# Kernel tuning notes

Hardware: AMD Instinct MI355X
Metric: run time of the kernel (lower is better)

The kernel has to match this reference:

```python
import jax, jax.numpy as jnp
import numpy as np

N_NODES = 100000
N_EDGES = 1600000
D_IN = 64
D_H = 64


def setup_inputs() -> dict:
    key = jax.random.key(0)
    ks = jax.random.split(key, 8)
    inp = {
        "in_feat": jax.random.normal(ks[0], (N_NODES, D_IN), dtype=jnp.float32),
        "src": jax.random.randint(ks[1], (N_EDGES,), 0, N_NODES, dtype=jnp.int64)
        if jax.config.jax_enable_x64
        else jax.random.randint(ks[1], (N_EDGES,), 0, N_NODES).astype(jnp.int32),
        "dst": jax.random.randint(ks[2], (N_EDGES,), 0, N_NODES).astype(jnp.int32),
        "W_self1": jax.random.normal(ks[3], (D_H, D_IN), dtype=jnp.float32) * 0.1,
        "W_neigh1": jax.random.normal(ks[4], (D_H, D_IN), dtype=jnp.float32) * 0.1,
        "b1": jnp.zeros((D_H,), dtype=jnp.float32),
        "W_self2": jax.random.normal(ks[5], (D_H, D_H), dtype=jnp.float32) * 0.1,
        "W_neigh2": jax.random.normal(ks[6], (D_H, D_H), dtype=jnp.float32) * 0.1,
        "b2": jnp.zeros((D_H,), dtype=jnp.float32),
    }
    inp["src"] = inp["src"].astype(jnp.int32)
    return inp


def _sage_mean(x, src, dst, W_self, W_neigh, b, n_nodes):
    # mean aggregation over incoming edges: gather src feats, segment-sum at dst
    msg_sum = jax.ops.segment_sum(x[src], dst, num_segments=n_nodes)  # [N, D]
    deg = jax.ops.segment_sum(jnp.ones_like(dst, dtype=x.dtype), dst, num_segments=n_nodes)
    h_neigh = msg_sum / jnp.maximum(deg, 1.0)[:, None]
    # DGL SAGEConv: fc_self(h) + fc_neigh(h_neigh) + bias
    return x @ W_self.T + h_neigh @ W_neigh.T + b


def reference(in_feat, src, dst, W_self1, W_neigh1, b1, W_self2, W_neigh2, b2):
    n = in_feat.shape[0]
    h = _sage_mean(in_feat, src, dst, W_self1, W_neigh1, b1, n)
    # dropout in eval mode is identity; then relu
    h = jax.nn.relu(h)
    h = _sage_mean(h, src, dst, W_self2, W_neigh2, b2, n)
    return h
```

## Files before the change

### kernel.cpp

```cpp
#include <hip/hip_runtime.h>

#define NN 100000
#define NE 1600000
#define NROWS 100032
#define CAP 48
#define ZOFF (NN * 64)
#define NRANGE 12500
#define SCAT_GROUPS 8
#define SCAT_CHUNKS 196
#define SCAT_EPB 8192
#define SCAT_BLKS (SCAT_GROUPS * SCAT_CHUNKS)
#define CAST_BLKS 6250
#define WCAT_BLKS 64
#define ZCUR_BLKS 391
#define AGG_BLKS 1563

typedef __attribute__((ext_vector_type(8))) short short8;
typedef __attribute__((ext_vector_type(4))) float float4v;
typedef __attribute__((ext_vector_type(4))) int int4v;

__device__ inline unsigned short f2bf(float f)
{
    union { float f; unsigned u; } v; v.f = f;
    unsigned r = v.u + 0x7FFF + ((v.u >> 16) & 1);
    return (unsigned short)(r >> 16);
}
__device__ inline float bf2f(unsigned short h)
{
    union { unsigned u; float f; } v; v.u = ((unsigned)h) << 16; return v.f;
}

__global__ __launch_bounds__(256) void prepA_kernel(
    const float* __restrict__ x,
    const float* __restrict__ Ws1, const float* __restrict__ Wn1,
    const float* __restrict__ Ws2, const float* __restrict__ Wn2,
    unsigned short* __restrict__ XF,
    unsigned short* __restrict__ W1, unsigned short* __restrict__ W2,
    int* __restrict__ cur)
{
    const int b = blockIdx.x;
    const int tid = threadIdx.x;
    if (b < CAST_BLKS) {
        int t = b * 256 + tid;
        int n = t >> 4;
        int k4 = (t & 15) * 4;
        float4v v = __builtin_nontemporal_load(
            (const float4v*)(x + (size_t)n * 64 + k4));
        ushort4 o;
        o.x = f2bf(v[0]); o.y = f2bf(v[1]); o.z = f2bf(v[2]); o.w = f2bf(v[3]);
        *(ushort4*)(XF + (size_t)n * 64 + k4) = o;
    } else if (b < CAST_BLKS + WCAT_BLKS) {
        int id = (b - CAST_BLKS) * 256 + tid;
        int l = id >> 13;
        int r = id & 8191;
        int o = r >> 7, k = r & 127;
        const float* Ws = l ? Ws2 : Ws1;
        const float* Wn = l ? Wn2 : Wn1;
        float v = (k < 64) ? Ws[o * 64 + k] : Wn[o * 64 + (k - 64)];
        (l ? W2 : W1)[r] = f2bf(v);
    } else if (b < CAST_BLKS + WCAT_BLKS + 1) {
        ushort4 z; z.x = 0; z.y = 0; z.z = 0; z.w = 0;
        for (int i = tid; i < 512; i += 256)
            *(ushort4*)(XF + (size_t)NN * 64 + i * 4) = z;
    } else {
        int i = (b - CAST_BLKS - WCAT_BLKS - 1) * 256 + tid;
        if (i < NN) cur[i] = 0;
    }
}

__global__ __launch_bounds__(256) void scatter_kernel(
    const int* __restrict__ src, const int* __restrict__ dst,
    int* __restrict__ cur, int* __restrict__ colb)
{
    const int b = blockIdx.x;
    const int tid = threadIdx.x;
    const int g = b & 7;
    const int chunk = b >> 3;
    const int lo = g * NRANGE;
    const int hi = lo + NRANGE;
    const int base = chunk * SCAT_EPB;
    #pragma unroll
    for (int k = 0; k < 8; ++k) {
        int e = base + (k * 256 + tid) * 4;
        if (e < NE) {
            int4v s4 = __builtin_nontemporal_load((const int4v*)(src + e));
            int4v d4 = __builtin_nontemporal_load((const int4v*)(dst + e));
            int p;
            if (d4[0] >= lo && d4[0] < hi) {
                p = atomicAdd(&cur[d4[0]], 1);
                if (p < CAP) colb[(size_t)d4[0] * CAP + p] = s4[0] << 6;
            }
            if (d4[1] >= lo && d4[1] < hi) {
                p = atomicAdd(&cur[d4[1]], 1);
                if (p < CAP) colb[(size_t)d4[1] * CAP + p] = s4[1] << 6;
            }
            if (d4[2] >= lo && d4[2] < hi) {
                p = atomicAdd(&cur[d4[2]], 1);
                if (p < CAP) colb[(size_t)d4[2] * CAP + p] = s4[2] << 6;
            }
            if (d4[3] >= lo && d4[3] < hi) {
                p = atomicAdd(&cur[d4[3]], 1);
                if (p < CAP) colb[(size_t)d4[3] * CAP + p] = s4[3] << 6;
            }
        }
    }
}

template <int LAYER1>
__global__ __launch_bounds__(256) void aggdense_kernel(
    const unsigned short* __restrict__ XIN,
    const int* __restrict__ cur,
    const int* __restrict__ colb,
    const unsigned short* __restrict__ Wcat,
    const float* __restrict__ bias,
    unsigned short* __restrict__ xout,
    float* __restrict__ fout)
{
    __shared__ __align__(16) unsigned short HN[64 * 72];
    const int tid = threadIdx.x;
    const int wave = tid >> 6;
    const int lane = tid & 63;
    const int g = lane >> 4;
    const int q = lane & 15;
    const int nbase = blockIdx.x * 64 + wave * 16;

    int cntv = (lane < 16 && nbase + lane < NN) ? cur[nbase + lane] : 0;

    int cnt_nx = __shfl(cntv, 0, 64);
    int cc_nx = min(cnt_nx, CAP);
    int ci_nx = (nbase < NN && lane < cc_nx) ? colb[(size_t)nbase * CAP + lane] : ZOFF;

    for (int i = 0; i < 16; ++i) {
        int n = nbase + i;
        int cnt = cnt_nx, cc = cc_nx, ci = ci_nx;
        if (i < 15) {
            cnt_nx = __shfl(cntv, i + 1, 64);
            cc_nx = min(cnt_nx, CAP);
            ci_nx = ((n + 1) < NN && lane < cc_nx)
                      ? colb[(size_t)(n + 1) * CAP + lane] : ZOFF;
        }
        if (n < NN) {
            float a0 = 0.f, a1 = 0.f, a2 = 0.f, a3 = 0.f;
            for (int t = 0; t < cc; t += 16) {
                int i0 = __shfl(ci, t + g, 64);
                int i1 = __shfl(ci, t + 4 + g, 64);
                int i2 = __shfl(ci, t + 8 + g, 64);
                int i3 = __shfl(ci, t + 12 + g, 64);
                ushort4 v0 = *(const ushort4*)(XIN + i0 + q * 4);
                ushort4 v1 = *(const ushort4*)(XIN + i1 + q * 4);
                ushort4 v2 = *(const ushort4*)(XIN + i2 + q * 4);
                ushort4 v3 = *(const ushort4*)(XIN + i3 + q * 4);
                a0 += bf2f(v0.x) + bf2f(v1.x) + bf2f(v2.x) + bf2f(v3.x);
                a1 += bf2f(v0.y) + bf2f(v1.y) + bf2f(v2.y) + bf2f(v3.y);
                a2 += bf2f(v0.z) + bf2f(v1.z) + bf2f(v2.z) + bf2f(v3.z);
                a3 += bf2f(v0.w) + bf2f(v1.w) + bf2f(v2.w) + bf2f(v3.w);
            }
            a0 += __shfl_xor(a0, 16, 64); a0 += __shfl_xor(a0, 32, 64);
            a1 += __shfl_xor(a1, 16, 64); a1 += __shfl_xor(a1, 32, 64);
            a2 += __shfl_xor(a2, 16, 64); a2 += __shfl_xor(a2, 32, 64);
            a3 += __shfl_xor(a3, 16, 64); a3 += __shfl_xor(a3, 32, 64);
            float rdeg = 1.0f / fmaxf((float)cnt, 1.0f);
            if (g == 0) {
                ushort4 o;
                o.x = f2bf(a0 * rdeg); o.y = f2bf(a1 * rdeg);
                o.z = f2bf(a2 * rdeg); o.w = f2bf(a3 * rdeg);
                *(ushort4*)(&HN[(wave * 16 + i) * 72 + q * 4]) = o;
            }
        }
    }
    __syncthreads();

    const int mrow = lane & 15;
    const int kb = lane >> 4;
    const int row0 = nbase;

    short8 a[4];
    {
        const short* ax = (const short*)XIN + (size_t)(row0 + mrow) * 64 + kb * 8;
        const short* ah = (const short*)HN + (wave * 16 + mrow) * 72 + kb * 8;
        a[0] = *(const short8*)(ax);
        a[1] = *(const short8*)(ax + 32);
        a[2] = *(const short8*)(ah);
        a[3] = *(const short8*)(ah + 32);
    }

    float4v acc[4];
    #pragma unroll
    for (int c = 0; c < 4; ++c) acc[c] = (float4v){0.f, 0.f, 0.f, 0.f};

    #pragma unroll
    for (int c = 0; c < 4; ++c) {
        const short* brow = (const short*)Wcat + (c * 16 + mrow) * 128 + kb * 8;
        #pragma unroll
        for (int i = 0; i < 4; ++i) {
            short8 bfr = *(const short8*)(brow + i * 32);
            acc[c] = __builtin_amdgcn_mfma_f32_16x16x32_bf16(a[i], bfr, acc[c], 0, 0, 0);
        }
    }

    const int rbase = row0 + (lane >> 4) * 4;
    #pragma unroll
    for (int c = 0; c < 4; ++c) {
        int o = c * 16 + mrow;
        float bv = bias[o];
        #pragma unroll
        for (int r = 0; r < 4; ++r) {
            int node = rbase + r;
            float val = acc[c][r] + bv;
            if (LAYER1) {
                float h = (node < NN) ? fmaxf(val, 0.f) : 0.f;
                xout[(size_t)node * 64 + o] = f2bf(h);
            } else {
                if (node < NN) fout[(size_t)node * 64 + o] = val;
            }
        }
    }
}

extern "C" void kernel_launch(void* const* d_in, const int* in_sizes, int n_in,
                              void* d_out, int out_size, void* d_ws, size_t ws_size,
                              hipStream_t stream)
{
    const float* in_feat = (const float*)d_in[0];
    const int*   src     = (const int*)d_in[1];
    const int*   dst     = (const int*)d_in[2];
    const float* Ws1     = (const float*)d_in[3];
    const float* Wn1     = (const float*)d_in[4];
    const float* b1      = (const float*)d_in[5];
    const float* Ws2     = (const float*)d_in[6];
    const float* Wn2     = (const float*)d_in[7];
    const float* b2      = (const float*)d_in[8];
    float* out = (float*)d_out;

    int* cur  = (int*)d_ws;
    int* colb = cur + NN;
    unsigned short* XF = (unsigned short*)(colb + (size_t)NN * CAP);
    unsigned short* H1 = XF + (size_t)NROWS * 64;
    unsigned short* W1 = H1 + (size_t)NROWS * 64;
    unsigned short* W2 = W1 + 8192;

    prepA_kernel<<<CAST_BLKS + WCAT_BLKS + 1 + ZCUR_BLKS, 256, 0, stream>>>(
        in_feat, Ws1, Wn1, Ws2, Wn2, XF, W1, W2, cur);

    scatter_kernel<<<SCAT_BLKS, 256, 0, stream>>>(src, dst, cur, colb);

    aggdense_kernel<1><<<AGG_BLKS, 256, 0, stream>>>(
        XF, cur, colb, W1, b1, H1, nullptr);

    aggdense_kernel<0><<<AGG_BLKS, 256, 0, stream>>>(
        H1, cur, colb, W2, b2, nullptr, out);
}
```

Measured before the change: 260.9 us.

## Merge scatter with cast kernel and halve nodes per aggregation block

Zeroing of the degree counters moves into its own small kernel, and the edge scatter runs in the same launch as the feature/weight bf16 cast, so the scatter and cast overlap instead of running as two serial launches. The aggregation kernel now handles 32 nodes per block (8 per wave) with twice as many blocks. This is meant to improve load balance and latency hiding for the irregular gather. Only two of the four waves do the MFMA dense step, leaving half the waves idle in that phase. Bounds checks are dropped because 100000 divides evenly by 32.

Measured after the change: 251.7 us. 3.5% less time.

```diff
diff --git a/kernel.cpp b/kernel.cpp
--- a/kernel.cpp
+++ b/kernel.cpp
@@ -13,7 +13,7 @@
 #define CAST_BLKS 6250
 #define WCAT_BLKS 64
 #define ZCUR_BLKS 391
-#define AGG_BLKS 1563
+#define AGG_BLKS 3125
 
 typedef __attribute__((ext_vector_type(8))) short short8;
 typedef __attribute__((ext_vector_type(4))) float float4v;
@@ -30,18 +30,56 @@
     union { unsigned u; float f; } v; v.u = ((unsigned)h) << 16; return v.f;
 }
 
-__global__ __launch_bounds__(256) void prepA_kernel(
+__global__ __launch_bounds__(256) void zero_kernel(int* __restrict__ cur)
+{
+    int i = blockIdx.x * 256 + threadIdx.x;
+    if (i < NN) cur[i] = 0;
+}
+
+__global__ __launch_bounds__(256) void prep_kernel(
     const float* __restrict__ x,
     const float* __restrict__ Ws1, const float* __restrict__ Wn1,
     const float* __restrict__ Ws2, const float* __restrict__ Wn2,
-    unsigned short* __restrict__ XF,
+    const int* __restrict__ src, const int* __restrict__ dst,
+    unsigned short* __restrict__ XF, unsigned short* __restrict__ H1,
     unsigned short* __restrict__ W1, unsigned short* __restrict__ W2,
-    int* __restrict__ cur)
+    int* __restrict__ cur, int* __restrict__ colb)
 {
     const int b = blockIdx.x;
     const int tid = threadIdx.x;
-    if (b < CAST_BLKS) {
-        int t = b * 256 + tid;
+    if (b < SCAT_BLKS) {
+        const int g = b & 7;
+        const int chunk = b >> 3;
+        const int lo = g * NRANGE;
+        const int hi = lo + NRANGE;
+        const int base = chunk * SCAT_EPB;
+        #pragma unroll
+        for (int k = 0; k < 8; ++k) {
+            int e = base + (k * 256 + tid) * 4;
+            if (e < NE) {
+                int4v s4 = __builtin_nontemporal_load((const int4v*)(src + e));
+                int4v d4 = __builtin_nontemporal_load((const int4v*)(dst + e));
+                int p;
+                if (d4[0] >= lo && d4[0] < hi) {
+                    p = atomicAdd(&cur[d4[0]], 1);
+                    if (p < CAP) colb[(size_t)d4[0] * CAP + p] = s4[0] << 6;
+                }
+                if (d4[1] >= lo && d4[1] < hi) {
+                    p = atomicAdd(&cur[d4[1]], 1);
+                    if (p < CAP) colb[(size_t)d4[1] * CAP + p] = s4[1] << 6;
+                }
+                if (d4[2] >= lo && d4[2] < hi) {
+                    p = atomicAdd(&cur[d4[2]], 1);
+                    if (p < CAP) colb[(size_t)d4[2] * CAP + p] = s4[2] << 6;
+                }
+                if (d4[3] >= lo && d4[3] < hi) {
+                    p = atomicAdd(&cur[d4[3]], 1);
+                    if (p < CAP) colb[(size_t)d4[3] * CAP + p] = s4[3] << 6;
+                }
+            }
+        }
+    } else if (b < SCAT_BLKS + CAST_BLKS) {
+        int t = (b - SCAT_BLKS) * 256 + tid;
         int n = t >> 4;
         int k4 = (t & 15) * 4;
         float4v v = __builtin_nontemporal_load(
@@ -49,8 +87,8 @@
         ushort4 o;
         o.x = f2bf(v[0]); o.y = f2bf(v[1]); o.z = f2bf(v[2]); o.w = f2bf(v[3]);
         *(ushort4*)(XF + (size_t)n * 64 + k4) = o;
-    } else if (b < CAST_BLKS + WCAT_BLKS) {
-        int id = (b - CAST_BLKS) * 256 + tid;
+    } else if (b < SCAT_BLKS + CAST_BLKS + WCAT_BLKS) {
+        int id = (b - SCAT_BLKS - CAST_BLKS) * 256 + tid;
         int l = id >> 13;
         int r = id & 8191;
         int o = r >> 7, k = r & 127;
@@ -58,50 +96,11 @@
         const float* Wn = l ? Wn2 : Wn1;
         float v = (k < 64) ? Ws[o * 64 + k] : Wn[o * 64 + (k - 64)];
         (l ? W2 : W1)[r] = f2bf(v);
-    } else if (b < CAST_BLKS + WCAT_BLKS + 1) {
-        ushort4 z; z.x = 0; z.y = 0; z.z = 0; z.w = 0;
-        for (int i = tid; i < 512; i += 256)
-            *(ushort4*)(XF + (size_t)NN * 64 + i * 4) = z;
     } else {
-        int i = (b - CAST_BLKS - WCAT_BLKS - 1) * 256 + tid;
-        if (i < NN) cur[i] = 0;
-    }
-}
-
-__global__ __launch_bounds__(256) void scatter_kernel(
-    const int* __restrict__ src, const int* __restrict__ dst,
-    int* __restrict__ cur, int* __restrict__ colb)
-{
-    const int b = blockIdx.x;
-    const int tid = threadIdx.x;
-    const int g = b & 7;
-    const int chunk = b >> 3;
-    const int lo = g * NRANGE;
-    const int hi = lo + NRANGE;
-    const int base = chunk * SCAT_EPB;
-    #pragma unroll
-    for (int k = 0; k < 8; ++k) {
-        int e = base + (k * 256 + tid) * 4;
-        if (e < NE) {
-            int4v s4 = __builtin_nontemporal_load((const int4v*)(src + e));
-            int4v d4 = __builtin_nontemporal_load((const int4v*)(dst + e));
-            int p;
-            if (d4[0] >= lo && d4[0] < hi) {
-                p = atomicAdd(&cur[d4[0]], 1);
-                if (p < CAP) colb[(size_t)d4[0] * CAP + p] = s4[0] << 6;
-            }
-            if (d4[1] >= lo && d4[1] < hi) {
-                p = atomicAdd(&cur[d4[1]], 1);
-                if (p < CAP) colb[(size_t)d4[1] * CAP + p] = s4[1] << 6;
-            }
-            if (d4[2] >= lo && d4[2] < hi) {
-                p = atomicAdd(&cur[d4[2]], 1);
-                if (p < CAP) colb[(size_t)d4[2] * CAP + p] = s4[2] << 6;
-            }
-            if (d4[3] >= lo && d4[3] < hi) {
-                p = atomicAdd(&cur[d4[3]], 1);
-                if (p < CAP) colb[(size_t)d4[3] * CAP + p] = s4[3] << 6;
-            }
+        if (tid < 32) {
+            ushort4 z; z.x = 0; z.y = 0; z.z = 0; z.w = 0;
+            unsigned short* base = (tid < 16) ? XF : H1;
+            *(ushort4*)(base + (size_t)NN * 64 + (tid & 15) * 4) = z;
         }
     }
 }
@@ -116,102 +115,100 @@
     unsigned short* __restrict__ xout,
     float* __restrict__ fout)
 {
-    __shared__ __align__(16) unsigned short HN[64 * 72];
+    __shared__ __align__(16) unsigned short HN[32 * 72];
     const int tid = threadIdx.x;
     const int wave = tid >> 6;
     const int lane = tid & 63;
     const int g = lane >> 4;
     const int q = lane & 15;
-    const int nbase = blockIdx.x * 64 + wave * 16;
-
-    int cntv = (lane < 16 && nbase + lane < NN) ? cur[nbase + lane] : 0;
+    const int nbase = blockIdx.x * 32 + wave * 8;
+
+    int cntv = (lane < 8) ? cur[nbase + lane] : 0;
 
     int cnt_nx = __shfl(cntv, 0, 64);
     int cc_nx = min(cnt_nx, CAP);
-    int ci_nx = (nbase < NN && lane < cc_nx) ? colb[(size_t)nbase * CAP + lane] : ZOFF;
-
-    for (int i = 0; i < 16; ++i) {
+    int ci_nx = (lane < cc_nx) ? colb[(size_t)nbase * CAP + lane] : ZOFF;
+
+    for (int i = 0; i < 8; ++i) {
         int n = nbase + i;
         int cnt = cnt_nx, cc = cc_nx, ci = ci_nx;
-        if (i < 15) {
+        if (i < 7) {
             cnt_nx = __shfl(cntv, i + 1, 64);
             cc_nx = min(cnt_nx, CAP);
-            ci_nx = ((n + 1) < NN && lane < cc_nx)
-                      ? colb[(size_t)(n + 1) * CAP + lane] : ZOFF;
-        }
-        if (n < NN) {
-            float a0 = 0.f, a1 = 0.f, a2 = 0.f, a3 = 0.f;
-            for (int t = 0; t < cc; t += 16) {
-                int i0 = __shfl(ci, t + g, 64);
-                int i1 = __shfl(ci, t + 4 + g, 64);
-                int i2 = __shfl(ci, t + 8 + g, 64);
-                int i3 = __shfl(ci, t + 12 + g, 64);
-                ushort4 v0 = *(const ushort4*)(XIN + i0 + q * 4);
-                ushort4 v1 = *(const ushort4*)(XIN + i1 + q * 4);
-                ushort4 v2 = *(const ushort4*)(XIN + i2 + q * 4);
-                ushort4 v3 = *(const ushort4*)(XIN + i3 + q * 4);
-                a0 += bf2f(v0.x) + bf2f(v1.x) + bf2f(v2.x) + bf2f(v3.x);
-                a1 += bf2f(v0.y) + bf2f(v1.y) + bf2f(v2.y) + bf2f(v3.y);
-                a2 += bf2f(v0.z) + bf2f(v1.z) + bf2f(v2.z) + bf2f(v3.z);
-                a3 += bf2f(v0.w) + bf2f(v1.w) + bf2f(v2.w) + bf2f(v3.w);
-            }
-            a0 += __shfl_xor(a0, 16, 64); a0 += __shfl_xor(a0, 32, 64);
-            a1 += __shfl_xor(a1, 16, 64); a1 += __shfl_xor(a1, 32, 64);
-            a2 += __shfl_xor(a2, 16, 64); a2 += __shfl_xor(a2, 32, 64);
-            a3 += __shfl_xor(a3, 16, 64); a3 += __shfl_xor(a3, 32, 64);
-            float rdeg = 1.0f / fmaxf((float)cnt, 1.0f);
-            if (g == 0) {
-                ushort4 o;
-                o.x = f2bf(a0 * rdeg); o.y = f2bf(a1 * rdeg);
-                o.z = f2bf(a2 * rdeg); o.w = f2bf(a3 * rdeg);
-                *(ushort4*)(&HN[(wave * 16 + i) * 72 + q * 4]) = o;
-            }
+            ci_nx = (lane < cc_nx) ? colb[(size_t)(n + 1) * CAP + lane] : ZOFF;
+        }
+        float a0 = 0.f, a1 = 0.f, a2 = 0.f, a3 = 0.f;
+        for (int t = 0; t < cc; t += 16) {
+            int i0 = __shfl(ci, t + g, 64);
+            int i1 = __shfl(ci, t + 4 + g, 64);
+            int i2 = __shfl(ci, t + 8 + g, 64);
+            int i3 = __shfl(ci, t + 12 + g, 64);
+            ushort4 v0 = *(const ushort4*)(XIN + i0 + q * 4);
+            ushort4 v1 = *(const ushort4*)(XIN + i1 + q * 4);
+            ushort4 v2 = *(const ushort4*)(XIN + i2 + q * 4);
+            ushort4 v3 = *(const ushort4*)(XIN + i3 + q * 4);
+            a0 += bf2f(v0.x) + bf2f(v1.x) + bf2f(v2.x) + bf2f(v3.x);
+            a1 += bf2f(v0.y) + bf2f(v1.y) + bf2f(v2.y) + bf2f(v3.y);
+            a2 += bf2f(v0.z) + bf2f(v1.z) + bf2f(v2.z) + bf2f(v3.z);
+            a3 += bf2f(v0.w) + bf2f(v1.w) + bf2f(v2.w) + bf2f(v3.w);
+        }
+        a0 += __shfl_xor(a0, 16, 64); a0 += __shfl_xor(a0, 32, 64);
+        a1 += __shfl_xor(a1, 16, 64); a1 += __shfl_xor(a1, 32, 64);
+        a2 += __shfl_xor(a2, 16, 64); a2 += __shfl_xor(a2, 32, 64);
+        a3 += __shfl_xor(a3, 16, 64); a3 += __shfl_xor(a3, 32, 64);
+        float rdeg = 1.0f / fmaxf((float)cnt, 1.0f);
+        if (g == 0) {
+            ushort4 o;
+            o.x = f2bf(a0 * rdeg); o.y = f2bf(a1 * rdeg);
+            o.z = f2bf(a2 * rdeg); o.w = f2bf(a3 * rdeg);
+            *(ushort4*)(&HN[(wave * 8 + i) * 72 + q * 4]) = o;
         }
     }
     __syncthreads();
 
-    const int mrow = lane & 15;
-    const int kb = lane >> 4;
-    const int row0 = nbase;
-
-    short8 a[4];
-    {
-        const short* ax = (const short*)XIN + (size_t)(row0 + mrow) * 64 + kb * 8;
-        const short* ah = (const short*)HN + (wave * 16 + mrow) * 72 + kb * 8;
-        a[0] = *(const short8*)(ax);
-        a[1] = *(const short8*)(ax + 32);
-        a[2] = *(const short8*)(ah);
-        a[3] = *(const short8*)(ah + 32);
-    }
-
-    float4v acc[4];
-    #pragma unroll
-    for (int c = 0; c < 4; ++c) acc[c] = (float4v){0.f, 0.f, 0.f, 0.f};
-
-    #pragma unroll
-    for (int c = 0; c < 4; ++c) {
-        const short* brow = (const short*)Wcat + (c * 16 + mrow) * 128 + kb * 8;
-        #pragma unroll
-        for (int i = 0; i < 4; ++i) {
-            short8 bfr = *(const short8*)(brow + i * 32);
-            acc[c] = __builtin_amdgcn_mfma_f32_16x16x32_bf16(a[i], bfr, acc[c], 0, 0, 0);
-        }
-    }
-
-    const int rbase = row0 + (lane >> 4) * 4;
-    #pragma unroll
-    for (int c = 0; c < 4; ++c) {
-        int o = c * 16 + mrow;
-        float bv = bias[o];
-        #pragma unroll
-        for (int r = 0; r < 4; ++r) {
-            int node = rbase + r;
-            float val = acc[c][r] + bv;
-            if (LAYER1) {
-                float h = (node < NN) ? fmaxf(val, 0.f) : 0.f;
-                xout[(size_t)node * 64 + o] = f2bf(h);
-            } else {
-                if (node < NN) fout[(size_t)node * 64 + o] = val;
+    if (wave < 2) {
+        const int mrow = lane & 15;
+        const int kb = lane >> 4;
+        const int row0 = blockIdx.x * 32 + wave * 16;
+
+        short8 a[4];
+        {
+            const short* ax = (const short*)XIN + (size_t)(row0 + mrow) * 64 + kb * 8;
+            const short* ah = (const short*)HN + (wave * 16 + mrow) * 72 + kb * 8;
+            a[0] = *(const short8*)(ax);
+            a[1] = *(const short8*)(ax + 32);
+            a[2] = *(const short8*)(ah);
+            a[3] = *(const short8*)(ah + 32);
+        }
+
+        float4v acc[4];
+        #pragma unroll
+        for (int c = 0; c < 4; ++c) acc[c] = (float4v){0.f, 0.f, 0.f, 0.f};
+
+        #pragma unroll
+        for (int c = 0; c < 4; ++c) {
+            const short* brow = (const short*)Wcat + (c * 16 + mrow) * 128 + kb * 8;
+            #pragma unroll
+            for (int i = 0; i < 4; ++i) {
+                short8 bfr = *(const short8*)(brow + i * 32);
+                acc[c] = __builtin_amdgcn_mfma_f32_16x16x32_bf16(a[i], bfr, acc[c], 0, 0, 0);
+            }
+        }
+
+        const int rbase = row0 + kb * 4;
+        #pragma unroll
+        for (int c = 0; c < 4; ++c) {
+            int o = c * 16 + mrow;
+            float bv = bias[o];
+            #pragma unroll
+            for (int r = 0; r < 4; ++r) {
+                int node = rbase + r;
+                float val = acc[c][r] + bv;
+                if (LAYER1) {
+                    xout[(size_t)node * 64 + o] = f2bf(fmaxf(val, 0.f));
+                } else {
+                    fout[(size_t)node * 64 + o] = val;
+                }
             }
         }
     }
@@ -239,10 +236,10 @@
     unsigned short* W1 = H1 + (size_t)NROWS * 64;
     unsigned short* W2 = W1 + 8192;
 
-    prepA_kernel<<<CAST_BLKS + WCAT_BLKS + 1 + ZCUR_BLKS, 256, 0, stream>>>(
-        in_feat, Ws1, Wn1, Ws2, Wn2, XF, W1, W2, cur);
-
-    scatter_kernel<<<SCAT_BLKS, 256, 0, stream>>>(src, dst, cur, colb);
+    zero_kernel<<<ZCUR_BLKS, 256, 0, stream>>>(cur);
+
+    prep_kernel<<<SCAT_BLKS + CAST_BLKS + WCAT_BLKS + 1, 256, 0, stream>>>(
+        in_feat, Ws1, Wn1, Ws2, Wn2, src, dst, XF, H1, W1, W2, cur, colb);
 
     aggdense_kernel<1><<<AGG_BLKS, 256, 0, stream>>>(
         XF, cur, colb, W1, b1, H1, nullptr);
```
